# Optimization experiments

Measured on AMD Instinct MI355X. Metric: run time of the kernel, lower is better.

Reference implementation:

```python
import jax, jax.numpy as jnp
import numpy as np

S = 3136        # tokens (56x56 patch grid, single image segment -> full attention)
H = 16          # num_heads
D = 80          # head_dim (= head_dim_ori = PADDING_HEAD_DIM)
HID = H * D     # 1280
SCALE = 1.0 / float(np.sqrt(D))  # qkScale = 1/sqrt(head_dim_ori)


def _rope_tables(s, d, base=10000.0):
    # rotate_half style: cos/sin of shape [s, d], duplicated over the two halves
    half = d // 2
    inv_freq = 1.0 / (base ** (np.arange(0, half, dtype=np.float32) / half))
    freqs = np.outer(np.arange(s, dtype=np.float32), inv_freq)  # [s, d/2]
    emb = np.concatenate([freqs, freqs], axis=-1)               # [s, d]
    return jnp.asarray(np.cos(emb)), jnp.asarray(np.sin(emb))


def setup_inputs() -> dict:
    key = jax.random.key(0)
    ks = jax.random.split(key, 6)
    cos, sin = _rope_tables(S, D)
    return {
        "hidden_states": jax.random.normal(ks[0], (S, HID), jnp.float32),
        "x_norm": jax.random.normal(ks[1], (S, HID), jnp.float32),
        "qkv_w": jax.random.normal(ks[2], (3 * HID, HID), jnp.float32) * 0.02,
        "qkv_b": jax.random.normal(ks[3], (3 * HID,), jnp.float32) * 0.02,
        "proj_w": jax.random.normal(ks[4], (HID, HID), jnp.float32) * 0.02,
        "proj_b": jax.random.normal(ks[5], (HID,), jnp.float32) * 0.02,
        "cos": cos,
        "sin": sin,
    }


def _rotate_half(x):
    x1, x2 = jnp.split(x, 2, axis=-1)
    return jnp.concatenate([-x2, x1], axis=-1)


def reference(hidden_states, x_norm, qkv_w, qkv_b, proj_w, proj_b, cos, sin):
    # fused QKV linear (transposeB=True) + split into q,k,v along last dim
    qkv = x_norm @ qkv_w.T + qkv_b                      # [S, 3*HID]
    q, k, v = jnp.split(qkv, 3, axis=-1)                # each [S, HID]
    q = q.reshape(S, H, D)
    k = k.reshape(S, H, D)
    v = v.reshape(S, H, D)
    # inline RoPE on q and k (rotate_half over full head_dim)
    c = cos[:, None, :]; s = sin[:, None, :]           # [S,1,D]
    q = q * c + _rotate_half(q) * s
    k = k * c + _rotate_half(k) * s
    # full self-attention (PA_ENCODER, single segment = seq_len S)
    scores = jnp.einsum('shd,thd->hst', q, k) * SCALE   # [H,S,S]
    probs = jax.nn.softmax(scores, axis=-1)
    attn = jnp.einsum('hst,thd->shd', probs, v)         # [S,H,D]
    attn = attn.reshape(S, HID)
    # output projection + residual add
    out = attn @ proj_w.T + proj_b
    return hidden_states + out
```

## Files before the change

### kernel.cpp

```cpp
#include <hip/hip_runtime.h>
#include <hip/hip_bf16.h>

#define S_   3136
#define H_   16
#define D_   80
#define DP_  96
#define HID_ 1280

typedef short  bf16x8 __attribute__((ext_vector_type(8)));
typedef short  bf16x4 __attribute__((ext_vector_type(4)));
typedef float  f32x4  __attribute__((ext_vector_type(4)));

__device__ __forceinline__ float b2f(unsigned short u) {
    union { unsigned int i; float f; } c;
    c.i = ((unsigned int)u) << 16;
    return c.f;
}
__device__ __forceinline__ unsigned short f2b(float f) {
    union { unsigned int i; float f; } c;
    c.f = f;
    unsigned int x = c.i;
    unsigned int lsb = (x >> 16) & 1u;
    x += 0x7fffu + lsb;
    return (unsigned short)(x >> 16);
}
__device__ __forceinline__ unsigned int cvt_pk_bf16(float lo, float hi) {
    unsigned int r;
    asm("v_cvt_pk_bf16_f32 %0, %1, %2" : "=v"(r) : "v"(lo), "v"(hi));
    return r;
}

typedef const void __attribute__((address_space(1))) GAS;
typedef void __attribute__((address_space(3))) LAS;
__device__ __forceinline__ void gl16(const void* g, void* l) {
    __builtin_amdgcn_global_load_lds((GAS*)g, (LAS*)l, 16, 0, 0);
}

#define N4_X 1003520
#define N4_Q 1228800
#define N4_P 409600

__global__ __launch_bounds__(256)
void cast3_kernel(const float* __restrict__ x0, unsigned short* __restrict__ y0,
                  const float* __restrict__ x1, unsigned short* __restrict__ y1,
                  const float* __restrict__ x2, unsigned short* __restrict__ y2)
{
    int i = blockIdx.x * 256 + threadIdx.x;
    const float* src; unsigned short* dst;
    if (i < N4_X)               { src = x0; dst = y0; }
    else if (i < N4_X + N4_Q)   { src = x1; dst = y1; i -= N4_X; }
    else if (i < N4_X + N4_Q + N4_P) { src = x2; dst = y2; i -= N4_X + N4_Q; }
    else return;
    float4 v = ((const float4*)src)[i];
    ushort4 o;
    o.x = f2b(v.x); o.y = f2b(v.y); o.z = f2b(v.z); o.w = f2b(v.w);
    ((ushort4*)dst)[i] = o;
}

#define ASTR 40

__global__ __launch_bounds__(256)
void qkv_mfma_kernel(const unsigned short* __restrict__ Ab,
                     const unsigned short* __restrict__ Wb,
                     const float* __restrict__ bias,
                     unsigned short* __restrict__ qo, unsigned short* __restrict__ ko,
                     unsigned short* __restrict__ vtb)
{
    __shared__ __align__(16) short As[2][128][ASTR];
    __shared__ __align__(16) short Bs[2][128][ASTR];
    int m0 = blockIdx.x * 128;
    int n0 = blockIdx.y * 128;
    int t = threadIdx.x;
    int wave = t >> 6, lane = t & 63, lq = lane & 15, quad = lane >> 4;
    int wr = wave >> 1, wc = wave & 1;

    int r0  = t >> 2;
    int r1  = r0 + 64;
    int kc0 = (t & 3) << 3;
    const unsigned short* pa0 = Ab + (size_t)min(m0 + r0, S_ - 1) * HID_ + kc0;
    const unsigned short* pa1 = Ab + (size_t)min(m0 + r1, S_ - 1) * HID_ + kc0;
    const unsigned short* pb0 = Wb + (size_t)(n0 + r0) * HID_ + kc0;
    const unsigned short* pb1 = Wb + (size_t)(n0 + r1) * HID_ + kc0;

    const bf16x8* afp[2][4]; const bf16x8* bfp[2][4];
    #pragma unroll
    for (int s = 0; s < 2; ++s)
        #pragma unroll
        for (int i = 0; i < 4; ++i) {
            afp[s][i] = (const bf16x8*)&As[s][wr * 64 + i * 16 + lq][quad * 8];
            bfp[s][i] = (const bf16x8*)&Bs[s][wc * 64 + i * 16 + lq][quad * 8];
        }

    f32x4 acc[4][4];
    #pragma unroll
    for (int i = 0; i < 4; ++i)
        #pragma unroll
        for (int j = 0; j < 4; ++j) acc[i][j] = (f32x4){0.f, 0.f, 0.f, 0.f};

    bf16x8 va[2][2], vb[2][2];
    #pragma unroll
    for (int s = 0; s < 2; ++s) {
        va[s][0] = *(const bf16x8*)(pa0 + s * 32);
        va[s][1] = *(const bf16x8*)(pa1 + s * 32);
        vb[s][0] = *(const bf16x8*)(pb0 + s * 32);
        vb[s][1] = *(const bf16x8*)(pb1 + s * 32);
    }

    for (int kt = 0; kt < HID_; kt += 64) {
        __syncthreads();
        #pragma unroll
        for (int s = 0; s < 2; ++s) {
            *(bf16x8*)&As[s][r0][kc0] = va[s][0];
            *(bf16x8*)&As[s][r1][kc0] = va[s][1];
            *(bf16x8*)&Bs[s][r0][kc0] = vb[s][0];
            *(bf16x8*)&Bs[s][r1][kc0] = vb[s][1];
        }
        __syncthreads();
        if (kt + 64 < HID_) {
            #pragma unroll
            for (int s = 0; s < 2; ++s) {
                va[s][0] = *(const bf16x8*)(pa0 + kt + 64 + s * 32);
                va[s][1] = *(const bf16x8*)(pa1 + kt + 64 + s * 32);
                vb[s][0] = *(const bf16x8*)(pb0 + kt + 64 + s * 32);
                vb[s][1] = *(const bf16x8*)(pb1 + kt + 64 + s * 32);
            }
        }
        #pragma unroll
        for (int s = 0; s < 2; ++s) {
            bf16x8 af[4], bfr[4];
            #pragma unroll
            for (int i = 0; i < 4; ++i) af[i]  = *afp[s][i];
            #pragma unroll
            for (int j = 0; j < 4; ++j) bfr[j] = *bfp[s][j];
            #pragma unroll
            for (int i = 0; i < 4; ++i)
                #pragma unroll
                for (int j = 0; j < 4; ++j)
                    acc[i][j] = __builtin_amdgcn_mfma_f32_16x16x32_bf16(af[i], bfr[j], acc[i][j], 0, 0, 0);
        }
    }

    #pragma unroll
    for (int i = 0; i < 4; ++i)
        #pragma unroll
        for (int j = 0; j < 4; ++j)
            #pragma unroll
            for (int reg = 0; reg < 4; ++reg) {
                int row = m0 + wr * 64 + i * 16 + quad * 4 + reg;
                if (row >= S_) continue;
                int col = n0 + wc * 64 + j * 16 + lq;
                float val = acc[i][j][reg] + bias[col];
                int which = col / HID_;
                int rem   = col - which * HID_;
                int h     = rem / D_;
                int d     = rem - h * D_;
                if (which == 0)      qo[((size_t)h * S_ + row) * D_ + d] = f2b(val);
                else if (which == 1) ko[((size_t)h * S_ + row) * D_ + d] = f2b(val);
                else                 vtb[((size_t)h * D_ + d) * S_ + row] = f2b(val);
            }
}

__global__ __launch_bounds__(256)
void proj_mfma_kernel(const unsigned short* __restrict__ Ab,
                      const unsigned short* __restrict__ Wb,
                      const float* __restrict__ bias, const float* __restrict__ hidden,
                      float* __restrict__ out)
{
    __shared__ __align__(16) short As[64][ASTR];
    __shared__ __align__(16) short Bs[64][ASTR];
    int m0 = blockIdx.x * 64;
    int n0 = blockIdx.y * 64;
    int t = threadIdx.x;
    int wave = t >> 6, lane = t & 63, lq = lane & 15, quad = lane >> 4;
    int wr = wave >> 1, wc = wave & 1;

    int r  = t >> 2;
    int kc0 = (t & 3) << 3;
    const unsigned short* pa = Ab + (size_t)(m0 + r) * HID_ + kc0;
    const unsigned short* pb = Wb + (size_t)(n0 + r) * HID_ + kc0;
    short* sa = &As[r][kc0];
    short* sb = &Bs[r][kc0];

    const bf16x8* afp[2]; const bf16x8* bfp[2];
    #pragma unroll
    for (int i = 0; i < 2; ++i) {
        afp[i] = (const bf16x8*)&As[wr * 32 + i * 16 + lq][quad * 8];
        bfp[i] = (const bf16x8*)&Bs[wc * 32 + i * 16 + lq][quad * 8];
    }

    f32x4 acc[2][2];
    #pragma unroll
    for (int i = 0; i < 2; ++i)
        #pragma unroll
        for (int j = 0; j < 2; ++j) acc[i][j] = (f32x4){0.f, 0.f, 0.f, 0.f};

    bf16x8 va = *(const bf16x8*)(pa);
    bf16x8 vb = *(const bf16x8*)(pb);

    for (int kt = 0; kt < HID_; kt += 32) {
        __syncthreads();
        *(bf16x8*)sa = va;
        *(bf16x8*)sb = vb;
        __syncthreads();
        if (kt + 32 < HID_) {
            va = *(const bf16x8*)(pa + kt + 32);
            vb = *(const bf16x8*)(pb + kt + 32);
        }
        bf16x8 af[2], bfr[2];
        #pragma unroll
        for (int i = 0; i < 2; ++i) af[i]  = *afp[i];
        #pragma unroll
        for (int j = 0; j < 2; ++j) bfr[j] = *bfp[j];
        #pragma unroll
        for (int i = 0; i < 2; ++i)
            #pragma unroll
            for (int j = 0; j < 2; ++j)
                acc[i][j] = __builtin_amdgcn_mfma_f32_16x16x32_bf16(af[i], bfr[j], acc[i][j], 0, 0, 0);
    }

    #pragma unroll
    for (int i = 0; i < 2; ++i)
        #pragma unroll
        for (int j = 0; j < 2; ++j)
            #pragma unroll
            for (int reg = 0; reg < 4; ++reg) {
                int row = m0 + wr * 32 + i * 16 + quad * 4 + reg;
                int col = n0 + wc * 32 + j * 16 + lq;
                out[(size_t)row * HID_ + col] =
                    acc[i][j][reg] + bias[col] + hidden[(size_t)row * HID_ + col];
            }
}

__global__ void rope_kernel(const unsigned short* __restrict__ q, const unsigned short* __restrict__ k,
                            const float* __restrict__ cost, const float* __restrict__ sint,
                            unsigned short* __restrict__ qb, unsigned short* __restrict__ kb)
{
    const float QSCALE = 0.11180339887498949f * 1.4426950408889634f;
    int idx = blockIdx.x * 256 + threadIdx.x;
    const int total = H_ * S_ * 40;
    if (idx >= total) return;
    int d  = idx % 40;
    int hs = idx / 40;
    int s  = hs % S_;
    size_t base  = (size_t)hs * D_;
    size_t base9 = (size_t)hs * DP_;
    float c1 = cost[s * D_ + d];
    float s1 = sint[s * D_ + d];
    float c2 = cost[s * D_ + d + 40];
    float s2 = sint[s * D_ + d + 40];
    float x1 = b2f(q[base + d]), x2 = b2f(q[base + d + 40]);
    qb[base9 + d]      = f2b((x1 * c1 - x2 * s1) * QSCALE);
    qb[base9 + d + 40] = f2b((x2 * c2 + x1 * s2) * QSCALE);
    x1 = b2f(k[base + d]); x2 = b2f(k[base + d + 40]);
    kb[base9 + d]      = f2b(x1 * c1 - x2 * s1);
    kb[base9 + d + 40] = f2b(x2 * c2 + x1 * s2);
    if (d < 16) {
        qb[base9 + 80 + d] = 0;
        kb[base9 + 80 + d] = 0;
    }
}

__global__ __launch_bounds__(256)
void attn_kernel(const unsigned short* __restrict__ Qb,
                 const unsigned short* __restrict__ Kb,
                 const unsigned short* __restrict__ Vtb,
                 unsigned short* __restrict__ attnb)
{
    __shared__ __align__(16) unsigned char smem[53248];

    int h   = blockIdx.y;
    int qb0 = blockIdx.x * 64;
    int t      = threadIdx.x;
    int wave   = t >> 6;
    int lane   = t & 63;
    int lq     = lane & 15;
    int quad   = lane >> 4;
    int qh     = wave & 1;
    int stripe = wave >> 1;
    int Q0     = qb0 + qh * 32;
    int swz    = (lq & 7) << 4;

    bf16x8 qf[2][3];
    #pragma unroll
    for (int qt = 0; qt < 2; ++qt)
        #pragma unroll
        for (int kc = 0; kc < 3; ++kc)
            qf[qt][kc] = *(const bf16x8*)(Qb + ((size_t)h * S_ + Q0 + qt * 16 + lq) * DP_ + kc * 32 + quad * 8);

    f32x4 O[2][5];
    #pragma unroll
    for (int qt = 0; qt < 2; ++qt)
        #pragma unroll
        for (int dt = 0; dt < 5; ++dt) O[qt][dt] = (f32x4){0.f, 0.f, 0.f, 0.f};
    float l_acc[2] = {0.f, 0.f};

    const int NR = (S_ + 127) / 128;

    for (int r = 0; r < NR; ++r) {
        int kbase = r * 128;
        bool stv = (kbase + stripe * 64) < S_;

        if (stv) {
            #pragma unroll
            for (int ii = 0; ii < 8; ++ii) {
                int i  = wave * 8 + ii;
                int rb = (i & 15) * 4;
                int rl = rb + (lane >> 4);
                int kg = kbase + stripe * 64 + rl;
                const unsigned short* src = Kb + ((size_t)h * S_ + kg) * DP_
                                          + (((((lane & 15) * 16) ^ ((rl & 7) << 4))) >> 1);
                gl16(src, smem + stripe * 16384 + rb * 256);
            }
            #pragma unroll
            for (int jj = 0; jj < 5; ++jj) {
                int j  = wave * 5 + jj;
                int jl = j - stripe * 10;
                int db = jl * 8;
                int d  = db + (lane >> 3);
                int scol = kbase + stripe * 64 + (((((lane & 7) * 16) ^ ((d & 7) << 4))) >> 1);
                gl16(Vtb + (size_t)(h * D_ + d) * S_ + scol,
                     smem + 32768 + stripe * 10240 + db * 128);
            }
        }
        asm volatile("s_waitcnt vmcnt(0)" ::: "memory");
        __syncthreads();

        if (stv) {
            union PaU { bf16x8 v8; unsigned int d[4]; };
            PaU pa[2][2];

            #pragma unroll
            for (int kcp = 0; kcp < 2; ++kcp) {
                f32x4 sc[2][2];
                #pragma unroll
                for (int sub = 0; sub < 2; ++sub) {
                    int kt = kcp * 2 + sub;
                    const unsigned char* kb = smem + stripe * 16384 + (kt * 16 + lq) * 256;
                    bf16x8 kf0 = *(const bf16x8*)(kb + (((0 * 64 + quad * 16)) ^ swz));
                    bf16x8 kf1 = *(const bf16x8*)(kb + (((1 * 64 + quad * 16)) ^ swz));
                    bf16x8 kf2 = *(const bf16x8*)(kb + (((2 * 64 + quad * 16)) ^ swz));
                    #pragma unroll
                    for (int qt = 0; qt < 2; ++qt) {
                        f32x4 a = (f32x4){0.f, 0.f, 0.f, 0.f};
                        a = __builtin_amdgcn_mfma_f32_16x16x32_bf16(kf0, qf[qt][0], a, 0, 0, 0);
                        a = __builtin_amdgcn_mfma_f32_16x16x32_bf16(kf1, qf[qt][1], a, 0, 0, 0);
                        a = __builtin_amdgcn_mfma_f32_16x16x32_bf16(kf2, qf[qt][2], a, 0, 0, 0);
                        sc[qt][sub] = a;
                    }
                }
                #pragma unroll
                for (int qt = 0; qt < 2; ++qt) {
                    float e00 = exp2f(sc[qt][0][0]), e01 = exp2f(sc[qt][0][1]);
                    float e02 = exp2f(sc[qt][0][2]), e03 = exp2f(sc[qt][0][3]);
                    float e10 = exp2f(sc[qt][1][0]), e11 = exp2f(sc[qt][1][1]);
                    float e12 = exp2f(sc[qt][1][2]), e13 = exp2f(sc[qt][1][3]);
                    l_acc[qt] += ((e00 + e01) + (e02 + e03)) + ((e10 + e11) + (e12 + e13));
                    pa[qt][kcp].d[0] = cvt_pk_bf16(e00, e01);
                    pa[qt][kcp].d[1] = cvt_pk_bf16(e02, e03);
                    pa[qt][kcp].d[2] = cvt_pk_bf16(e10, e11);
                    pa[qt][kcp].d[3] = cvt_pk_bf16(e12, e13);
                }
            }

            #pragma unroll
            for (int kcp = 0; kcp < 2; ++kcp) {
                #pragma unroll
                for (int dt = 0; dt < 5; ++dt) {
                    const unsigned char* vb = smem + 32768 + stripe * 10240 + (dt * 16 + lq) * 128;
                    union { bf16x8 v8; bf16x4 v4[2]; } vv;
                    vv.v4[0] = *(const bf16x4*)(vb + (((kcp * 64 + quad * 8)) ^ swz));
                    vv.v4[1] = *(const bf16x4*)(vb + (((kcp * 64 + 32 + quad * 8)) ^ swz));
                    #pragma unroll
                    for (int qt = 0; qt < 2; ++qt)
                        O[qt][dt] = __builtin_amdgcn_mfma_f32_16x16x32_bf16(pa[qt][kcp].v8, vv.v8, O[qt][dt], 0, 0, 0);
                }
            }
        }
        __syncthreads();
    }

    float lr[2];
    #pragma unroll
    for (int qt = 0; qt < 2; ++qt) {
        float l = l_acc[qt];
        l += __shfl_xor(l, 16);
        l += __shfl_xor(l, 32);
        lr[qt] = l;
    }
    f32x4* Of = (f32x4*)smem;
    float* Lf = (float*)(smem + 20480);
    if (stripe == 1) {
        #pragma unroll
        for (int qt = 0; qt < 2; ++qt) {
            #pragma unroll
            for (int dt = 0; dt < 5; ++dt)
                Of[((qh * 2 + qt) * 5 + dt) * 64 + lane] = O[qt][dt];
            if (lane < 16) Lf[(qh * 2 + qt) * 16 + lane] = lr[qt];
        }
    }
    __syncthreads();
    if (stripe == 0) {
        #pragma unroll
        for (int qt = 0; qt < 2; ++qt) {
            float ltot = lr[qt] + Lf[(qh * 2 + qt) * 16 + lq];
            #pragma unroll
            for (int dt = 0; dt < 5; ++dt)
                O[qt][dt] += Of[((qh * 2 + qt) * 5 + dt) * 64 + lane];
            #pragma unroll
            for (int reg = 0; reg < 4; ++reg) {
                float l = __shfl(ltot, quad * 4 + reg, 16);
                float linv = 1.0f / l;
                int s = Q0 + qt * 16 + quad * 4 + reg;
                unsigned short* orow = attnb + (size_t)s * HID_ + h * D_;
                #pragma unroll
                for (int dt = 0; dt < 5; ++dt)
                    orow[dt * 16 + lq] = f2b(O[qt][dt][reg] * linv);
            }
        }
    }
}

extern "C" void kernel_launch(void* const* d_in, const int* in_sizes, int n_in,
                              void* d_out, int out_size, void* d_ws, size_t ws_size,
                              hipStream_t stream)
{
    const float* hidden = (const float*)d_in[0];
    const float* x_norm = (const float*)d_in[1];
    const float* qkv_w  = (const float*)d_in[2];
    const float* qkv_b  = (const float*)d_in[3];
    const float* proj_w = (const float*)d_in[4];
    const float* proj_b = (const float*)d_in[5];
    const float* cost   = (const float*)d_in[6];
    const float* sint   = (const float*)d_in[7];
    float* out = (float*)d_out;

    unsigned short* w      = (unsigned short*)d_ws;
    unsigned short* qbuf   = w;
    unsigned short* kbuf   = qbuf + 4014080;
    unsigned short* vtb    = kbuf + 4014080;
    unsigned short* kbb    = vtb + 4064256;
    unsigned short* xb     = kbb + 4816896;
    unsigned short* wqkvb  = xb + 4014080;
    unsigned short* wprojb = wqkvb + 4915200;
    unsigned short* qbb    = wqkvb;
    unsigned short* abuf   = qbuf;

    cast3_kernel<<<(N4_X + N4_Q + N4_P + 255) / 256, 256, 0, stream>>>(
        x_norm, xb, qkv_w, wqkvb, proj_w, wprojb);

    qkv_mfma_kernel<<<dim3(25, 30), 256, 0, stream>>>(xb, wqkvb, qkv_b, qbuf, kbuf, vtb);
    rope_kernel<<<(H_ * S_ * 40 + 255) / 256, 256, 0, stream>>>(qbuf, kbuf, cost, sint, qbb, kbb);
    attn_kernel<<<dim3(S_ / 64, H_), 256, 0, stream>>>(qbb, kbb, vtb, abuf);
    proj_mfma_kernel<<<dim3(49, 20), 256, 0, stream>>>(abuf, wprojb, proj_b, hidden, out);
}
```

Baseline: 326.5 us.

## Double-buffer K/V tiles in LDS to overlap global loads with MFMA compute

Restructures the attention key loop from a single 128-key round with serialized load-then-compute into 64-key tiles that are double-buffered in shared memory. The next tile's K/V loads are issued before computing on the current one, and there is one barrier per iteration instead of two. The two wave stripes now split each 64-key tile rather than each owning separate keys, and launch bounds request 3 blocks per CU. This hides global load latency at the cost of more iterations, a hardcoded loop count of 49, and possible register pressure.

```diff
diff --git a/kernel.cpp b/kernel.cpp
--- a/kernel.cpp
+++ b/kernel.cpp
@@ -260,13 +260,17 @@
     }
 }
 
-__global__ __launch_bounds__(256)
+#define KBUF_ 16384
+#define VBUF_ 10240
+#define BUF_  26624
+
+__global__ __launch_bounds__(256, 3)
 void attn_kernel(const unsigned short* __restrict__ Qb,
                  const unsigned short* __restrict__ Kb,
                  const unsigned short* __restrict__ Vtb,
                  unsigned short* __restrict__ attnb)
 {
-    __shared__ __align__(16) unsigned char smem[53248];
+    __shared__ __align__(16) unsigned char smem[2 * BUF_];
 
     int h   = blockIdx.y;
     int qb0 = blockIdx.x * 64;
@@ -294,90 +298,96 @@
         for (int dt = 0; dt < 5; ++dt) O[qt][dt] = (f32x4){0.f, 0.f, 0.f, 0.f};
     float l_acc[2] = {0.f, 0.f};
 
-    const int NR = (S_ + 127) / 128;
-
-    for (int r = 0; r < NR; ++r) {
-        int kbase = r * 128;
-        bool stv = (kbase + stripe * 64) < S_;
-
-        if (stv) {
-            #pragma unroll
-            for (int ii = 0; ii < 8; ++ii) {
-                int i  = wave * 8 + ii;
-                int rb = (i & 15) * 4;
-                int rl = rb + (lane >> 4);
-                int kg = kbase + stripe * 64 + rl;
-                const unsigned short* src = Kb + ((size_t)h * S_ + kg) * DP_
-                                          + (((((lane & 15) * 16) ^ ((rl & 7) << 4))) >> 1);
-                gl16(src, smem + stripe * 16384 + rb * 256);
+    const unsigned char* kS[4]; int kD[4];
+    #pragma unroll
+    for (int ii = 0; ii < 4; ++ii) {
+        int i  = wave * 4 + ii;
+        int rl = i * 4 + (lane >> 4);
+        kS[ii] = (const unsigned char*)(Kb + ((size_t)h * S_ + rl) * DP_)
+               + (((lane & 15) * 16) ^ ((rl & 7) << 4));
+        kD[ii] = i * 1024;
+    }
+    const unsigned char* vS[3]; int vD[3];
+    int nv = (wave < 2) ? 3 : 2;
+    #pragma unroll
+    for (int jj = 0; jj < 3; ++jj) {
+        int j = (jj < 2) ? (wave + jj * 4) : (8 + wave);
+        int d = j * 8 + (lane >> 3);
+        vS[jj] = (const unsigned char*)(Vtb + (size_t)(h * D_ + d) * S_)
+               + (((lane & 7) * 16) ^ ((d & 7) << 4));
+        vD[jj] = KBUF_ + j * 1024;
+    }
+
+    #define STAGE(bufoff, rr)                                                   \
+        do {                                                                    \
+            size_t kadv = (size_t)(rr) * (64 * DP_ * 2);                        \
+            size_t vadv = (size_t)(rr) * 128;                                   \
+            _Pragma("unroll")                                                   \
+            for (int ii = 0; ii < 4; ++ii)                                      \
+                gl16(kS[ii] + kadv, smem + (bufoff) + kD[ii]);                  \
+            _Pragma("unroll")                                                   \
+            for (int jj = 0; jj < 3; ++jj)                                      \
+                if (jj < nv) gl16(vS[jj] + vadv, smem + (bufoff) + vD[jj]);     \
+        } while (0)
+
+    STAGE(0, 0);
+    asm volatile("s_waitcnt vmcnt(0)" ::: "memory");
+    __syncthreads();
+
+    int cur = 0;
+    for (int r = 0; r < 49; ++r) {
+        if (r < 48) STAGE(cur ^ BUF_, r + 1);
+
+        const unsigned char* Kbase = smem + cur;
+        const unsigned char* Vbase = Kbase + KBUF_;
+
+        f32x4 sc[2][2];
+        #pragma unroll
+        for (int kt = 0; kt < 2; ++kt) {
+            const unsigned char* kbp = Kbase + (stripe * 32 + kt * 16 + lq) * 256;
+            bf16x8 kf0 = *(const bf16x8*)(kbp + ((  0 + quad * 16) ^ swz));
+            bf16x8 kf1 = *(const bf16x8*)(kbp + (( 64 + quad * 16) ^ swz));
+            bf16x8 kf2 = *(const bf16x8*)(kbp + ((128 + quad * 16) ^ swz));
+            #pragma unroll
+            for (int qt = 0; qt < 2; ++qt) {
+                f32x4 a = (f32x4){0.f, 0.f, 0.f, 0.f};
+                a = __builtin_amdgcn_mfma_f32_16x16x32_bf16(kf0, qf[qt][0], a, 0, 0, 0);
+                a = __builtin_amdgcn_mfma_f32_16x16x32_bf16(kf1, qf[qt][1], a, 0, 0, 0);
+                a = __builtin_amdgcn_mfma_f32_16x16x32_bf16(kf2, qf[qt][2], a, 0, 0, 0);
+                sc[qt][kt] = a;
             }
-            #pragma unroll
-            for (int jj = 0; jj < 5; ++jj) {
-                int j  = wave * 5 + jj;
-                int jl = j - stripe * 10;
-                int db = jl * 8;
-                int d  = db + (lane >> 3);
-                int scol = kbase + stripe * 64 + (((((lane & 7) * 16) ^ ((d & 7) << 4))) >> 1);
-                gl16(Vtb + (size_t)(h * D_ + d) * S_ + scol,
-                     smem + 32768 + stripe * 10240 + db * 128);
-            }
-        }
+        }
+
+        union PaU { bf16x8 v8; unsigned int d[4]; } pa[2];
+        #pragma unroll
+        for (int qt = 0; qt < 2; ++qt) {
+            float e00 = exp2f(sc[qt][0][0]), e01 = exp2f(sc[qt][0][1]);
+            float e02 = exp2f(sc[qt][0][2]), e03 = exp2f(sc[qt][0][3]);
+            float e10 = exp2f(sc[qt][1][0]), e11 = exp2f(sc[qt][1][1]);
+            float e12 = exp2f(sc[qt][1][2]), e13 = exp2f(sc[qt][1][3]);
+            l_acc[qt] += ((e00 + e01) + (e02 + e03)) + ((e10 + e11) + (e12 + e13));
+            pa[qt].d[0] = cvt_pk_bf16(e00, e01);
+            pa[qt].d[1] = cvt_pk_bf16(e02, e03);
+            pa[qt].d[2] = cvt_pk_bf16(e10, e11);
+            pa[qt].d[3] = cvt_pk_bf16(e12, e13);
+        }
+
+        #pragma unroll
+        for (int dt = 0; dt < 5; ++dt) {
+            const unsigned char* vbp = Vbase + (dt * 16 + lq) * 128;
+            union { bf16x8 v8; bf16x4 v4[2]; } vv;
+            vv.v4[0] = *(const bf16x4*)(vbp + ((stripe * 64 +      quad * 8) ^ swz));
+            vv.v4[1] = *(const bf16x4*)(vbp + ((stripe * 64 + 32 + quad * 8) ^ swz));
+            #pragma unroll
+            for (int qt = 0; qt < 2; ++qt)
+                O[qt][dt] = __builtin_amdgcn_mfma_f32_16x16x32_bf16(pa[qt].v8, vv.v8, O[qt][dt], 0, 0, 0);
+        }
+
         asm volatile("s_waitcnt vmcnt(0)" ::: "memory");
         __syncthreads();
-
-        if (stv) {
-            union PaU { bf16x8 v8; unsigned int d[4]; };
-            PaU pa[2][2];
-
-            #pragma unroll
-            for (int kcp = 0; kcp < 2; ++kcp) {
-                f32x4 sc[2][2];
-                #pragma unroll
-                for (int sub = 0; sub < 2; ++sub) {
-                    int kt = kcp * 2 + sub;
-                    const unsigned char* kb = smem + stripe * 16384 + (kt * 16 + lq) * 256;
-                    bf16x8 kf0 = *(const bf16x8*)(kb + (((0 * 64 + quad * 16)) ^ swz));
-                    bf16x8 kf1 = *(const bf16x8*)(kb + (((1 * 64 + quad * 16)) ^ swz));
-                    bf16x8 kf2 = *(const bf16x8*)(kb + (((2 * 64 + quad * 16)) ^ swz));
-                    #pragma unroll
-                    for (int qt = 0; qt < 2; ++qt) {
-                        f32x4 a = (f32x4){0.f, 0.f, 0.f, 0.f};
-                        a = __builtin_amdgcn_mfma_f32_16x16x32_bf16(kf0, qf[qt][0], a, 0, 0, 0);
-                        a = __builtin_amdgcn_mfma_f32_16x16x32_bf16(kf1, qf[qt][1], a, 0, 0, 0);
-                        a = __builtin_amdgcn_mfma_f32_16x16x32_bf16(kf2, qf[qt][2], a, 0, 0, 0);
-                        sc[qt][sub] = a;
-                    }
-                }
-                #pragma unroll
-                for (int qt = 0; qt < 2; ++qt) {
-                    float e00 = exp2f(sc[qt][0][0]), e01 = exp2f(sc[qt][0][1]);
-                    float e02 = exp2f(sc[qt][0][2]), e03 = exp2f(sc[qt][0][3]);
-                    float e10 = exp2f(sc[qt][1][0]), e11 = exp2f(sc[qt][1][1]);
-                    float e12 = exp2f(sc[qt][1][2]), e13 = exp2f(sc[qt][1][3]);
-                    l_acc[qt] += ((e00 + e01) + (e02 + e03)) + ((e10 + e11) + (e12 + e13));
-                    pa[qt][kcp].d[0] = cvt_pk_bf16(e00, e01);
-                    pa[qt][kcp].d[1] = cvt_pk_bf16(e02, e03);
-                    pa[qt][kcp].d[2] = cvt_pk_bf16(e10, e11);
-                    pa[qt][kcp].d[3] = cvt_pk_bf16(e12, e13);
-                }
-            }
-
-            #pragma unroll
-            for (int kcp = 0; kcp < 2; ++kcp) {
-                #pragma unroll
-                for (int dt = 0; dt < 5; ++dt) {
-                    const unsigned char* vb = smem + 32768 + stripe * 10240 + (dt * 16 + lq) * 128;
-                    union { bf16x8 v8; bf16x4 v4[2]; } vv;
-                    vv.v4[0] = *(const bf16x4*)(vb + (((kcp * 64 + quad * 8)) ^ swz));
-                    vv.v4[1] = *(const bf16x4*)(vb + (((kcp * 64 + 32 + quad * 8)) ^ swz));
-                    #pragma unroll
-                    for (int qt = 0; qt < 2; ++qt)
-                        O[qt][dt] = __builtin_amdgcn_mfma_f32_16x16x32_bf16(pa[qt][kcp].v8, vv.v8, O[qt][dt], 0, 0, 0);
-                }
-            }
-        }
-        __syncthreads();
-    }
+        cur ^= BUF_;
+    }
+    #undef STAGE
 
     float lr[2];
     #pragma unroll
```

Result: faster. 315.9 us (-3.2%).
